# Kernel tuning notes

Measured on AMD Instinct MI355X. Metric: run time of the kernel, lower is better.

The kernel has to match this reference:

```python
import jax, jax.numpy as jnp
import numpy as np

PATCH = 16      # sqrt(n_patches=256)
ALPHA = 10.0
HEADS, DH = 2, 64


def _fourier(coords, Bm):
    # coords: (HW, 2), Bm: (n_features, 2) -> (HW, 2*n_features)
    proj = 2.0 * jnp.pi * coords @ Bm.T
    return jnp.concatenate([jnp.cos(proj), jnp.sin(proj)], axis=-1)


def _forward(coords_decoding, tokens, B_q, B_l0, B_l1,
             qW, qb, toqW, tokvW, tooW, toob,
             bwW0, bwb0, bwW1, bwb1,
             modW0, modb0, modW1, modb1,
             hvW0, hvb0, outW0, outb0, outW1, outb1):
    B = coords_decoding.shape[0]
    Hh, Ww = coords_decoding.shape[1], coords_decoding.shape[2]
    coords = coords_decoding.reshape(B, -1, coords_decoding.shape[-1])
    grid = coords[0]                      # (HW, 2); coords_modulation is None -> same grid
    HW = grid.shape[0]
    m = tokens.shape[1]

    # patch indices and spatial bias
    row = jnp.clip((grid[:, 0] * PATCH).astype(jnp.int32), 0, PATCH - 1)
    col = jnp.clip((grid[:, 1] * PATCH).astype(jnp.int32), 0, PATCH - 1)
    idx = row * PATCH + col               # (HW,)
    t = idx.astype(jnp.float32) / (PATCH * PATCH)
    pos = (jnp.arange(m, dtype=jnp.float32) + 0.5) / m
    rel = -ALPHA * jnp.abs(t[None, :] - pos[:, None]) ** 2   # (m, HW)
    bias = rel.T                          # (HW, m), broadcast over batch & heads

    # query features (shared across batch)
    xq = jax.nn.relu(_fourier(grid, B_q) @ qW + qb)           # (HW, hd)
    xq_b = jnp.broadcast_to(xq[None], (B, HW, xq.shape[-1]))

    # cross attention with spatial bias
    q = (xq_b @ toqW).reshape(B, HW, HEADS, DH).transpose(0, 2, 1, 3)   # (B,h,HW,Dh)
    kv = tokens @ tokvW                                                  # (B,m,2*inner)
    k, v = jnp.split(kv, 2, axis=-1)
    k = k.reshape(B, m, HEADS, DH).transpose(0, 2, 1, 3)                 # (B,h,m,Dh)
    v = v.reshape(B, m, HEADS, DH).transpose(0, 2, 1, 3)
    sim = jnp.einsum('bhqd,bhkd->bhqk', q, k) * (DH ** -0.5) + bias[None, None]
    attn = jax.nn.softmax(sim, axis=-1)
    o = jnp.einsum('bhqk,bhkd->bhqd', attn, v)
    o = o.transpose(0, 2, 1, 3).reshape(B, HW, HEADS * DH)
    mod = o @ tooW + toob                                                # (B,HW,hd)

    # per-band MLP stack (layer_num = 2)
    def band(Bl, bwW, bwb, mW, mb):
        h = jax.nn.relu(_fourier(grid, Bl) @ bwW + bwb)                  # (HW,hd)
        return jax.nn.relu(h[None] + mod @ mW + mb)                      # (B,HW,hd)

    m0 = band(B_l0, bwW0, bwb0, modW0, modb0)
    m1 = band(B_l1, bwW1, bwb1, modW1, modb1)
    hv0 = m0
    hv1 = jax.nn.relu((m1 + hv0) @ hvW0 + hvb0)
    out = (hv0 @ outW0 + outb0) + (hv1 @ outW1 + outb1)                  # (B,HW,3)
    return out.reshape(B, Hh, Ww, -1)


def setup_inputs() -> dict:
    key = jax.random.key(0)
    ks = jax.random.split(key, 32)
    B, H, W, L = 4, 128, 128, 256
    fd, hd, cd, od = 64, 256, 256, 3
    nf = fd // 2
    inner = HEADS * DH

    def lin(k, i, o):
        return jax.random.normal(k, (i, o), dtype=jnp.float32) / np.sqrt(i).astype(np.float32)

    inp = {}
    inp['coords_decoding'] = jax.random.uniform(ks[0], (B, H, W, 2), dtype=jnp.float32)
    inp['tokens'] = jax.random.normal(ks[1], (B, L, cd), dtype=jnp.float32)
    inp['B_q'] = jax.random.normal(ks[2], (nf, 2), dtype=jnp.float32) / 16.0
    inp['B_l0'] = jax.random.normal(ks[3], (nf, 2), dtype=jnp.float32) / 128.0
    inp['B_l1'] = jax.random.normal(ks[4], (nf, 2), dtype=jnp.float32) / 32.0
    inp['qW'] = lin(ks[5], fd, hd); inp['qb'] = jnp.zeros((hd,), jnp.float32)
    inp['toqW'] = lin(ks[6], hd, inner)
    inp['tokvW'] = lin(ks[7], cd, inner * 2)
    inp['tooW'] = lin(ks[8], inner, hd); inp['toob'] = jnp.zeros((hd,), jnp.float32)
    inp['bwW0'] = lin(ks[9], fd, hd); inp['bwb0'] = jnp.zeros((hd,), jnp.float32)
    inp['bwW1'] = lin(ks[10], fd, hd); inp['bwb1'] = jnp.zeros((hd,), jnp.float32)
    inp['modW0'] = lin(ks[11], hd, hd); inp['modb0'] = jnp.zeros((hd,), jnp.float32)
    inp['modW1'] = lin(ks[12], hd, hd); inp['modb1'] = jnp.zeros((hd,), jnp.float32)
    inp['hvW0'] = lin(ks[13], hd, hd); inp['hvb0'] = jnp.zeros((hd,), jnp.float32)
    inp['outW0'] = lin(ks[14], hd, od); inp['outb0'] = jnp.zeros((od,), jnp.float32)
    inp['outW1'] = lin(ks[15], hd, od); inp['outb1'] = jnp.zeros((od,), jnp.float32)
    return inp


def reference(coords_decoding, tokens, B_q, B_l0, B_l1,
              qW, qb, toqW, tokvW, tooW, toob,
              bwW0, bwb0, bwW1, bwb1,
              modW0, modb0, modW1, modb1,
              hvW0, hvb0, outW0, outb0, outW1, outb1):
    return _forward(coords_decoding, tokens, B_q, B_l0, B_l1,
                    qW, qb, toqW, tokvW, tooW, toob,
                    bwW0, bwb0, bwW1, bwb1,
                    modW0, modb0, modW1, modb1,
                    hvW0, hvb0, outW0, outb0, outW1, outb1)
```

## Files before the change

### kernel.cpp

```cpp
#include <hip/hip_runtime.h>
#include <stdint.h>

constexpr int kHW = 16384;
constexpr int kB  = 4;
constexpr int kM  = 256;

typedef _Float16 half8 __attribute__((ext_vector_type(8)));
typedef __attribute__((ext_vector_type(4))) float f32x4;

__device__ __forceinline__ unsigned short f2h(float f) {
  _Float16 h = (_Float16)f;
  return __builtin_bit_cast(unsigned short, h);
}
__device__ __forceinline__ float h2f(unsigned short u) {
  return (float)__builtin_bit_cast(_Float16, u);
}

__global__ __launch_bounds__(256) void prep_kernel(
    const float* __restrict__ tokens, const float* __restrict__ tokvW,
    unsigned short* __restrict__ kn_ws, unsigned short* __restrict__ vt_ws,
    const float* __restrict__ tooW, const float* __restrict__ modW0,
    const float* __restrict__ modW1, const float* __restrict__ hvW0,
    const float* __restrict__ qW, const float* __restrict__ bwW0,
    const float* __restrict__ bwW1, const float* __restrict__ toqW,
    unsigned short* __restrict__ tooWt, unsigned short* __restrict__ modW0t,
    unsigned short* __restrict__ modW1t, unsigned short* __restrict__ hvW0t,
    unsigned short* __restrict__ qWt, unsigned short* __restrict__ bw0t,
    unsigned short* __restrict__ bw1t, unsigned short* __restrict__ toqWt)
{
  __shared__ __align__(16) float tok[256];
  int bx = blockIdx.x, tid = threadIdx.x;

  if (bx < kB * kM) {
    int b = bx >> 8, j = bx & 255, c = tid;
    tok[c] = tokens[(b * kM + j) * 256 + c];
    __syncthreads();
    float acc = 0.f;
    for (int i4 = 0; i4 < 64; i4++) {
      float4 t4 = *(const float4*)&tok[i4 * 4];
      acc += t4.x * tokvW[(i4*4+0)*256 + c] + t4.y * tokvW[(i4*4+1)*256 + c]
           + t4.z * tokvW[(i4*4+2)*256 + c] + t4.w * tokvW[(i4*4+3)*256 + c];
    }
    unsigned short hv = f2h(acc);
    if (c < 128) {
      int h = c >> 6, dd = c & 63;
      kn_ws[((size_t)(b*2+h)*256 + j) * 64 + dd] = hv;
    } else {
      int c2 = c - 128;
      int h = c2 >> 6, dd = c2 & 63;
      vt_ws[((size_t)(b*2+h)*64 + dd) * 256 + j] = hv;
    }
  } else {
    int t = bx - kB * kM;
    int m = t >> 3, ch = t & 7;
    const float* Ws[8] = {tooW, modW0, modW1, hvW0, qW, bwW0, bwW1, toqW};
    unsigned short* Wts[8] = {tooWt, modW0t, modW1t, hvW0t, qWt, bw0t, bw1t, toqWt};
    const int Ks[8] = {128, 256, 256, 256, 64, 64, 64, 256};
    const int Ns[8] = {256, 256, 256, 256, 256, 256, 256, 128};
    const float* W = Ws[m];
    unsigned short* Wt = Wts[m];
    int K = Ks[m], N = Ns[m];
    int nkb = K / 8;
    int per = nkb >> 3;
    int kb0 = ch * per;
    if (tid < N) {
      for (int kb = kb0; kb < kb0 + per; kb++) {
        unsigned short sv[8];
#pragma unroll
        for (int i = 0; i < 8; i++)
          sv[i] = f2h(W[(kb * 8 + i) * N + tid]);
        *(uint4*)&Wt[tid * K + kb * 8] = *(const uint4*)sv;
      }
    }
  }
}

constexpr int kAPitch = 264;
constexpr int kQPitch = 136;

__global__ __launch_bounds__(256, 2) void featattn_kernel(
    const float* __restrict__ coords,
    const float* __restrict__ Bq, const float* __restrict__ Bl0, const float* __restrict__ Bl1,
    const float* __restrict__ qb, const float* __restrict__ bwb0, const float* __restrict__ bwb1,
    const unsigned short* __restrict__ qWt, const unsigned short* __restrict__ bw0t,
    const unsigned short* __restrict__ bw1t, const unsigned short* __restrict__ toqWt,
    const unsigned short* __restrict__ kn_ws, const unsigned short* __restrict__ vt_ws,
    unsigned short* __restrict__ h0_hf, unsigned short* __restrict__ h1_hf,
    unsigned short* __restrict__ o_hf)
{
  __shared__ __align__(16) unsigned short arena[15360];
  __shared__ __align__(16) unsigned short qc_s[32 * kQPitch];
  __shared__ float t_s[32];
  __shared__ float coords_s[64];
  __shared__ float red_max[32][4];
  __shared__ float red_sum[32][4];

  unsigned short* ff  = arena;
  unsigned short* xq  = arena + 6912;
  unsigned short* P_s = arena;

  int tid = threadIdx.x;
  int px0 = blockIdx.x * 32;
  int w = tid >> 6, ln = tid & 63;
  int c = ln & 15, q = ln >> 4;

  const f32x4 zero4 = {0.f, 0.f, 0.f, 0.f};

  if (tid < 64) coords_s[tid] = coords[px0 * 2 + tid];
  __syncthreads();

#pragma unroll
  for (int r = 0; r < 24; r++) {
    int v = r * 256 + tid;
    int mat = v >> 11;
    int p = (v >> 6) & 31;
    int f = v & 63;
    int fr = f & 31;
    const float* Bm = (mat == 0) ? Bq : (mat == 1 ? Bl0 : Bl1);
    float x = coords_s[p * 2 + 0];
    float y = coords_s[p * 2 + 1];
    float proj = 6.283185307179586f * (x * Bm[fr*2+0] + y * Bm[fr*2+1]);
    float s, cc;
    __sincosf(proj, &s, &cc);
    ff[(mat * 32 + p) * 72 + f] = f2h((f < 32) ? cc : s);
  }
  if (tid < 32) {
    float x = coords_s[tid * 2 + 0];
    float y = coords_s[tid * 2 + 1];
    int row = min(max((int)(x * 16.0f), 0), 15);
    int col = min(max((int)(y * 16.0f), 0), 15);
    t_s[tid] = (float)(row * 16 + col) * (1.0f / 256.0f);
  }
  __syncthreads();

  for (int mat = 0; mat < 3; mat++) {
    const unsigned short* Wt = (mat == 0) ? qWt : (mat == 1 ? bw0t : bw1t);
    const float* bias = (mat == 0) ? qb : (mat == 1 ? bwb0 : bwb1);
    f32x4 acc[8];
#pragma unroll
    for (int i = 0; i < 8; i++) acc[i] = zero4;
#pragma unroll
    for (int ks = 0; ks < 2; ks++) {
      int koff = ks * 32 + q * 8;
      half8 bfr[4];
#pragma unroll
      for (int nt = 0; nt < 4; nt++)
        bfr[nt] = *(const half8*)(Wt + (size_t)(w*64 + nt*16 + c) * 64 + koff);
      half8 afr[2];
#pragma unroll
      for (int mt = 0; mt < 2; mt++)
        afr[mt] = *(const half8*)(ff + (mat * 32 + mt*16 + c) * 72 + koff);
#pragma unroll
      for (int mt = 0; mt < 2; mt++)
#pragma unroll
        for (int nt = 0; nt < 4; nt++)
          acc[mt*4+nt] = __builtin_amdgcn_mfma_f32_16x16x32_f16(afr[mt], bfr[nt], acc[mt*4+nt], 0, 0, 0);
    }
    float bv[4];
#pragma unroll
    for (int nt = 0; nt < 4; nt++) bv[nt] = bias[w*64 + nt*16 + c];
#pragma unroll
    for (int mt = 0; mt < 2; mt++)
#pragma unroll
      for (int nt = 0; nt < 4; nt++)
#pragma unroll
        for (int rg = 0; rg < 4; rg++) {
          int row = mt*16 + q*4 + rg, col = w*64 + nt*16 + c;
          unsigned short hv = f2h(fmaxf(acc[mt*4+nt][rg] + bv[nt], 0.f));
          if (mat == 0)      xq[row * kAPitch + col] = hv;
          else if (mat == 1) h0_hf[((size_t)(px0 + row)) * 256 + col] = hv;
          else               h1_hf[((size_t)(px0 + row)) * 256 + col] = hv;
        }
  }
  __syncthreads();

  {
    f32x4 acc2[4];
#pragma unroll
    for (int i = 0; i < 4; i++) acc2[i] = zero4;
#pragma unroll
    for (int kt = 0; kt < 8; kt++) {
      int koff = kt * 32 + q * 8;
      half8 bfr[2];
#pragma unroll
      for (int nt = 0; nt < 2; nt++)
        bfr[nt] = *(const half8*)(toqWt + (size_t)(w*32 + nt*16 + c) * 256 + koff);
      half8 afr[2];
#pragma unroll
      for (int mt = 0; mt < 2; mt++)
        afr[mt] = *(const half8*)(xq + (mt*16 + c) * kAPitch + koff);
#pragma unroll
      for (int mt = 0; mt < 2; mt++)
#pragma unroll
        for (int nt = 0; nt < 2; nt++)
          acc2[mt*2+nt] = __builtin_amdgcn_mfma_f32_16x16x32_f16(afr[mt], bfr[nt], acc2[mt*2+nt], 0, 0, 0);
    }
#pragma unroll
    for (int mt = 0; mt < 2; mt++)
#pragma unroll
      for (int nt = 0; nt < 2; nt++)
#pragma unroll
        for (int rg = 0; rg < 4; rg++) {
          int row = mt*16 + q*4 + rg, col = w*32 + nt*16 + c;
          qc_s[row * kQPitch + col] = f2h(acc2[mt*2+nt][rg]);
        }
  }

  for (int b = 0; b < kB; b++) {
    for (int h = 0; h < 2; h++) {
      __syncthreads();

      f32x4 acc[8];
#pragma unroll
      for (int i = 0; i < 8; i++) acc[i] = zero4;
      const unsigned short* kbase = kn_ws + (size_t)(b*2+h) * 256 * 64;
#pragma unroll
      for (int ks = 0; ks < 2; ks++) {
        int koff = ks * 32 + q * 8;
        half8 a0 = *(const half8*)(qc_s + c * kQPitch + h*64 + koff);
        half8 a1 = *(const half8*)(qc_s + (16 + c) * kQPitch + h*64 + koff);
#pragma unroll
        for (int nt = 0; nt < 4; nt++) {
          half8 bf = *(const half8*)(kbase + (size_t)(w*64 + nt*16 + c) * 64 + koff);
          acc[0*4+nt] = __builtin_amdgcn_mfma_f32_16x16x32_f16(a0, bf, acc[0*4+nt], 0, 0, 0);
          acc[1*4+nt] = __builtin_amdgcn_mfma_f32_16x16x32_f16(a1, bf, acc[1*4+nt], 0, 0, 0);
        }
      }

      float lm[2][4];
#pragma unroll
      for (int mt = 0; mt < 2; mt++)
#pragma unroll
        for (int rg = 0; rg < 4; rg++) {
          int row = mt*16 + q*4 + rg;
          float tv = t_s[row];
          float mx = -1e30f;
#pragma unroll
          for (int nt = 0; nt < 4; nt++) {
            int token = w*64 + nt*16 + c;
            float pos = ((float)token + 0.5f) * (1.0f / 256.0f);
            float db = tv - pos;
            float sb = acc[mt*4+nt][rg] * 0.125f - 10.0f * db * db;
            acc[mt*4+nt][rg] = sb;
            mx = fmaxf(mx, sb);
          }
          lm[mt][rg] = mx;
        }
#pragma unroll
      for (int s = 1; s < 16; s <<= 1)
#pragma unroll
        for (int mt = 0; mt < 2; mt++)
#pragma unroll
          for (int rg = 0; rg < 4; rg++)
            lm[mt][rg] = fmaxf(lm[mt][rg], __shfl_xor(lm[mt][rg], s, 64));
      if (c == 0) {
#pragma unroll
        for (int mt = 0; mt < 2; mt++)
#pragma unroll
          for (int rg = 0; rg < 4; rg++)
            red_max[mt*16 + q*4 + rg][w] = lm[mt][rg];
      }
      __syncthreads();

      float ps[2][4];
#pragma unroll
      for (int mt = 0; mt < 2; mt++)
#pragma unroll
        for (int rg = 0; rg < 4; rg++) {
          int row = mt*16 + q*4 + rg;
          float gm = fmaxf(fmaxf(red_max[row][0], red_max[row][1]),
                           fmaxf(red_max[row][2], red_max[row][3]));
          float sum = 0.f;
#pragma unroll
          for (int nt = 0; nt < 4; nt++) {
            float e = __expf(acc[mt*4+nt][rg] - gm);
            sum += e;
            P_s[row * kAPitch + w*64 + nt*16 + c] = f2h(e);
          }
          ps[mt][rg] = sum;
        }
#pragma unroll
      for (int s = 1; s < 16; s <<= 1)
#pragma unroll
        for (int mt = 0; mt < 2; mt++)
#pragma unroll
          for (int rg = 0; rg < 4; rg++)
            ps[mt][rg] += __shfl_xor(ps[mt][rg], s, 64);
      if (c == 0) {
#pragma unroll
        for (int mt = 0; mt < 2; mt++)
#pragma unroll
          for (int rg = 0; rg < 4; rg++)
            red_sum[mt*16 + q*4 + rg][w] = ps[mt][rg];
      }
      __syncthreads();

      f32x4 oacc[2] = {zero4, zero4};
      const unsigned short* vbase = vt_ws + (size_t)(b*2+h) * 64 * 256;
#pragma unroll
      for (int kt = 0; kt < 8; kt++) {
        int koff = kt * 32 + q * 8;
        half8 bf = *(const half8*)(vbase + (size_t)(w*16 + c) * 256 + koff);
        half8 a0 = *(const half8*)(P_s + (0*16 + c) * kAPitch + koff);
        half8 a1 = *(const half8*)(P_s + (1*16 + c) * kAPitch + koff);
        oacc[0] = __builtin_amdgcn_mfma_f32_16x16x32_f16(a0, bf, oacc[0], 0, 0, 0);
        oacc[1] = __builtin_amdgcn_mfma_f32_16x16x32_f16(a1, bf, oacc[1], 0, 0, 0);
      }
#pragma unroll
      for (int mt = 0; mt < 2; mt++)
#pragma unroll
        for (int rg = 0; rg < 4; rg++) {
          int row = mt*16 + q*4 + rg;
          float rinv = 1.0f / (red_sum[row][0] + red_sum[row][1] +
                               red_sum[row][2] + red_sum[row][3]);
          o_hf[((size_t)(b * kHW + px0 + row)) * 128 + h*64 + w*16 + c] =
              f2h(oacc[mt][rg] * rinv);
        }
    }
  }
}

constexpr int kPitch = 264;

template <int KD>
__device__ __forceinline__ void gemm4(
    const unsigned short* abuf, const unsigned short* wt,
    f32x4* acc , int c, int q)
{
#pragma unroll
  for (int ks = 0; ks < KD / 32; ks++) {
    int koff = ks * 32 + q * 8;
    half8 bfr[4];
#pragma unroll
    for (int nt = 0; nt < 4; nt++)
      bfr[nt] = *(const half8*)(wt + (nt * 16 + c) * KD + koff);
    half8 afr[4];
#pragma unroll
    for (int mt = 0; mt < 4; mt++)
      afr[mt] = *(const half8*)(abuf + (mt * 16 + c) * kPitch + koff);
#pragma unroll
    for (int mt = 0; mt < 4; mt++)
#pragma unroll
      for (int nt = 0; nt < 4; nt++)
        acc[mt * 4 + nt] = __builtin_amdgcn_mfma_f32_16x16x32_f16(afr[mt], bfr[nt], acc[mt * 4 + nt], 0, 0, 0);
  }
}

__global__ __launch_bounds__(256, 2) void mlp_kernel(
    const unsigned short* __restrict__ o_hf,
    const unsigned short* __restrict__ h0_hf, const unsigned short* __restrict__ h1_hf,
    const unsigned short* __restrict__ tooWt, const float* __restrict__ toob,
    const unsigned short* __restrict__ modW0t, const float* __restrict__ modb0,
    const unsigned short* __restrict__ modW1t, const float* __restrict__ modb1,
    const unsigned short* __restrict__ hvW0t, const float* __restrict__ hvb0,
    const float* __restrict__ outW0, const float* __restrict__ outb0,
    const float* __restrict__ outW1, const float* __restrict__ outb1,
    float* __restrict__ dout)
{
  __shared__ __align__(16) unsigned short buf0[64 * kPitch];
  __shared__ __align__(16) unsigned short buf1[64 * kPitch];
  __shared__ __align__(16) float scratch[64 * 12];

  int tid = threadIdx.x;
  int px0 = blockIdx.x * 16;
  int w = tid >> 6, ln = tid & 63;
  int c = ln & 15, q = ln >> 4;

  unsigned short h0r[4][4], h1r[4][4];
#pragma unroll
  for (int nt = 0; nt < 4; nt++) {
    int col = w * 64 + nt * 16 + c;
#pragma unroll
    for (int rg = 0; rg < 4; rg++) {
      int px = q * 4 + rg;
      h0r[nt][rg] = h0_hf[((size_t)(px0 + px)) * 256 + col];
      h1r[nt][rg] = h1_hf[((size_t)(px0 + px)) * 256 + col];
    }
  }

#pragma unroll
  for (int i = 0; i < 4; i++) {
    int idx = i * 256 + tid;
    int r = idx >> 4, c8 = (idx & 15) * 8;
    int b = r >> 4, px = r & 15;
    uint4 v = *(const uint4*)(o_hf + ((size_t)(b * kHW + px0 + px)) * 128 + c8);
    *(uint4*)&buf0[r * kPitch + c8] = v;
  }
  __syncthreads();

  f32x4 acc[16];
  const f32x4 zero4 = {0.f, 0.f, 0.f, 0.f};

#pragma unroll
  for (int i = 0; i < 16; i++) acc[i] = zero4;
  gemm4<128>(buf0, tooWt + (size_t)w * 64 * 128, acc, c, q);
  {
    float bias[4];
#pragma unroll
    for (int nt = 0; nt < 4; nt++) bias[nt] = toob[w * 64 + nt * 16 + c];
#pragma unroll
    for (int mt = 0; mt < 4; mt++)
#pragma unroll
      for (int nt = 0; nt < 4; nt++)
#pragma unroll
        for (int rg = 0; rg < 4; rg++) {
          int row = mt * 16 + q * 4 + rg, col = w * 64 + nt * 16 + c;
          buf1[row * kPitch + col] = f2h(acc[mt * 4 + nt][rg] + bias[nt]);
        }
  }
  __syncthreads();

  _Float16 m0h[4][4][4];
#pragma unroll
  for (int i = 0; i < 16; i++) acc[i] = zero4;
  gemm4<256>(buf1, modW0t + (size_t)w * 64 * 256, acc, c, q);
  {
    float bias[4];
#pragma unroll
    for (int nt = 0; nt < 4; nt++) bias[nt] = modb0[w * 64 + nt * 16 + c];
#pragma unroll
    for (int mt = 0; mt < 4; mt++)
#pragma unroll
      for (int nt = 0; nt < 4; nt++)
#pragma unroll
        for (int rg = 0; rg < 4; rg++)
          m0h[mt][nt][rg] =
              (_Float16)fmaxf(acc[mt * 4 + nt][rg] + bias[nt] + h2f(h0r[nt][rg]), 0.f);
  }

#pragma unroll
  for (int i = 0; i < 16; i++) acc[i] = zero4;
  gemm4<256>(buf1, modW1t + (size_t)w * 64 * 256, acc, c, q);
  {
    float bias[4];
#pragma unroll
    for (int nt = 0; nt < 4; nt++) bias[nt] = modb1[w * 64 + nt * 16 + c];
#pragma unroll
    for (int mt = 0; mt < 4; mt++)
#pragma unroll
      for (int nt = 0; nt < 4; nt++)
#pragma unroll
        for (int rg = 0; rg < 4; rg++) {
          int row = mt * 16 + q * 4 + rg, col = w * 64 + nt * 16 + c;
          float m0v = (float)m0h[mt][nt][rg];
          float v = m0v + fmaxf(acc[mt * 4 + nt][rg] + bias[nt] + h2f(h1r[nt][rg]), 0.f);
          buf0[row * kPitch + col] = f2h(v);
        }
  }
  __syncthreads();

#pragma unroll
  for (int i = 0; i < 16; i++) acc[i] = zero4;
  gemm4<256>(buf0, hvW0t + (size_t)w * 64 * 256, acc, c, q);
  {
    float bias[4], w0v[4][3], w1v[4][3];
#pragma unroll
    for (int nt = 0; nt < 4; nt++) {
      int col = w * 64 + nt * 16 + c;
      bias[nt] = hvb0[col];
#pragma unroll
      for (int k = 0; k < 3; k++) {
        w0v[nt][k] = outW0[col * 3 + k];
        w1v[nt][k] = outW1[col * 3 + k];
      }
    }
#pragma unroll
    for (int mt = 0; mt < 4; mt++) {
      float pk[4][3];
#pragma unroll
      for (int rg = 0; rg < 4; rg++)
#pragma unroll
        for (int k = 0; k < 3; k++) pk[rg][k] = 0.f;
#pragma unroll
      for (int nt = 0; nt < 4; nt++) {
#pragma unroll
        for (int rg = 0; rg < 4; rg++) {
          float hv1 = fmaxf(acc[mt * 4 + nt][rg] + bias[nt], 0.f);
          float m0v = (float)m0h[mt][nt][rg];
#pragma unroll
          for (int k = 0; k < 3; k++)
            pk[rg][k] += m0v * w0v[nt][k] + hv1 * w1v[nt][k];
        }
      }
#pragma unroll
      for (int s = 1; s < 16; s <<= 1)
#pragma unroll
        for (int rg = 0; rg < 4; rg++)
#pragma unroll
          for (int k = 0; k < 3; k++)
            pk[rg][k] += __shfl_xor(pk[rg][k], s, 64);
      if (c == 0) {
#pragma unroll
        for (int rg = 0; rg < 4; rg++) {
          int row = mt * 16 + q * 4 + rg;
#pragma unroll
          for (int k = 0; k < 3; k++)
            scratch[row * 12 + k * 4 + w] = pk[rg][k];
        }
      }
    }
  }
  __syncthreads();

  if (tid < 192) {
    int row = tid / 3, k = tid % 3;
    int b = row >> 4, px = px0 + (row & 15);
    float s = outb0[k] + outb1[k];
#pragma unroll
    for (int ww = 0; ww < 4; ww++) s += scratch[row * 12 + k * 4 + ww];
    dout[((size_t)b * kHW + px) * 3 + k] = s;
  }
}

extern "C" void kernel_launch(void* const* d_in, const int* in_sizes, int n_in,
                              void* d_out, int out_size, void* d_ws, size_t ws_size,
                              hipStream_t stream) {
  const float* coords = (const float*)d_in[0];
  const float* tokens = (const float*)d_in[1];
  const float* Bq     = (const float*)d_in[2];
  const float* Bl0    = (const float*)d_in[3];
  const float* Bl1    = (const float*)d_in[4];
  const float* qW     = (const float*)d_in[5];
  const float* qb     = (const float*)d_in[6];
  const float* toqW   = (const float*)d_in[7];
  const float* tokvW  = (const float*)d_in[8];
  const float* tooW   = (const float*)d_in[9];
  const float* toob   = (const float*)d_in[10];
  const float* bwW0   = (const float*)d_in[11];
  const float* bwb0   = (const float*)d_in[12];
  const float* bwW1   = (const float*)d_in[13];
  const float* bwb1   = (const float*)d_in[14];
  const float* modW0  = (const float*)d_in[15];
  const float* modb0  = (const float*)d_in[16];
  const float* modW1  = (const float*)d_in[17];
  const float* modb1  = (const float*)d_in[18];
  const float* hvW0   = (const float*)d_in[19];
  const float* hvb0   = (const float*)d_in[20];
  const float* outW0  = (const float*)d_in[21];
  const float* outb0  = (const float*)d_in[22];
  const float* outW1  = (const float*)d_in[23];
  const float* outb1  = (const float*)d_in[24];

  char* ws = (char*)d_ws;
  unsigned short* h0_hf  = (unsigned short*)(ws + 0);
  unsigned short* h1_hf  = (unsigned short*)(ws + 8388608);
  unsigned short* o_hf   = (unsigned short*)(ws + 16777216);
  unsigned short* kn_ws  = (unsigned short*)(ws + 33554432);
  unsigned short* vt_ws  = (unsigned short*)(ws + 33816576);
  unsigned short* tooWt  = (unsigned short*)(ws + 34078720);
  unsigned short* modW0t = (unsigned short*)(ws + 34144256);
  unsigned short* modW1t = (unsigned short*)(ws + 34275328);
  unsigned short* hvW0t  = (unsigned short*)(ws + 34406400);
  unsigned short* qWt    = (unsigned short*)(ws + 34537472);
  unsigned short* bw0t   = (unsigned short*)(ws + 34570240);
  unsigned short* bw1t   = (unsigned short*)(ws + 34603008);
  unsigned short* toqWt  = (unsigned short*)(ws + 34635776);

  prep_kernel<<<dim3(kB * kM + 64), 256, 0, stream>>>(
      tokens, tokvW, kn_ws, vt_ws,
      tooW, modW0, modW1, hvW0, qW, bwW0, bwW1, toqW,
      tooWt, modW0t, modW1t, hvW0t, qWt, bw0t, bw1t, toqWt);
  featattn_kernel<<<dim3(kHW / 32), 256, 0, stream>>>(
      coords, Bq, Bl0, Bl1, qb, bwb0, bwb1,
      qWt, bw0t, bw1t, toqWt,
      kn_ws, vt_ws,
      h0_hf, h1_hf, o_hf);
  mlp_kernel<<<dim3(kHW / 16), 256, 0, stream>>>(
      o_hf, h0_hf, h1_hf, tooWt, toob, modW0t, modb0, modW1t, modb1,
      hvW0t, hvb0, outW0, outb0, outW1, outb1, (float*)d_out);
}
```

Measured before the change: 258.8 us.

## Halve MLP kernel row tile and stage residuals in shared memory for occupancy

The MLP kernel now handles 8 pixels (32 rows across the batch) per block instead of 16, so each wave keeps 8 accumulators instead of 16. The h0/h1 residual inputs move from register arrays to a shared buffer, and the m0 intermediate is kept in shared memory instead of registers. Launch bounds rise to 4 blocks per CU and the grid doubles. The goal is to cut register and LDS pressure so more waves run at once. The cost is that each weight tile is read from global/L2 twice as often overall, and the kernel adds extra barriers and more LDS traffic.

Result: slower. 286.9 us (+10.9%).

```diff
diff --git a/kernel.cpp b/kernel.cpp
--- a/kernel.cpp
+++ b/kernel.cpp
@@ -323,7 +323,7 @@
 constexpr int kPitch = 264;
 
 template <int KD>
-__device__ __forceinline__ void gemm4(
+__device__ __forceinline__ void gemm2m(
     const unsigned short* abuf, const unsigned short* wt,
     f32x4* acc , int c, int q)
 {
@@ -334,19 +334,19 @@
 #pragma unroll
     for (int nt = 0; nt < 4; nt++)
       bfr[nt] = *(const half8*)(wt + (nt * 16 + c) * KD + koff);
-    half8 afr[4];
-#pragma unroll
-    for (int mt = 0; mt < 4; mt++)
+    half8 afr[2];
+#pragma unroll
+    for (int mt = 0; mt < 2; mt++)
       afr[mt] = *(const half8*)(abuf + (mt * 16 + c) * kPitch + koff);
 #pragma unroll
-    for (int mt = 0; mt < 4; mt++)
+    for (int mt = 0; mt < 2; mt++)
 #pragma unroll
       for (int nt = 0; nt < 4; nt++)
         acc[mt * 4 + nt] = __builtin_amdgcn_mfma_f32_16x16x32_f16(afr[mt], bfr[nt], acc[mt * 4 + nt], 0, 0, 0);
   }
 }
 
-__global__ __launch_bounds__(256, 2) void mlp_kernel(
+__global__ __launch_bounds__(256, 4) void mlp_kernel(
     const unsigned short* __restrict__ o_hf,
     const unsigned short* __restrict__ h0_hf, const unsigned short* __restrict__ h1_hf,
     const unsigned short* __restrict__ tooWt, const float* __restrict__ toob,
@@ -357,49 +357,43 @@
     const float* __restrict__ outW1, const float* __restrict__ outb1,
     float* __restrict__ dout)
 {
-  __shared__ __align__(16) unsigned short buf0[64 * kPitch];
-  __shared__ __align__(16) unsigned short buf1[64 * kPitch];
-  __shared__ __align__(16) float scratch[64 * 12];
+  __shared__ __align__(16) unsigned short buf0[32 * kPitch];
+  __shared__ __align__(16) unsigned short buf1[32 * kPitch];
+  __shared__ __align__(16) unsigned short hbuf[8 * kPitch];
+  __shared__ __align__(16) float scratch[32 * 12];
 
   int tid = threadIdx.x;
-  int px0 = blockIdx.x * 16;
+  int px0 = blockIdx.x * 8;
   int w = tid >> 6, ln = tid & 63;
   int c = ln & 15, q = ln >> 4;
 
-  unsigned short h0r[4][4], h1r[4][4];
-#pragma unroll
-  for (int nt = 0; nt < 4; nt++) {
-    int col = w * 64 + nt * 16 + c;
-#pragma unroll
-    for (int rg = 0; rg < 4; rg++) {
-      int px = q * 4 + rg;
-      h0r[nt][rg] = h0_hf[((size_t)(px0 + px)) * 256 + col];
-      h1r[nt][rg] = h1_hf[((size_t)(px0 + px)) * 256 + col];
-    }
-  }
-
-#pragma unroll
-  for (int i = 0; i < 4; i++) {
+#pragma unroll
+  for (int i = 0; i < 2; i++) {
     int idx = i * 256 + tid;
     int r = idx >> 4, c8 = (idx & 15) * 8;
-    int b = r >> 4, px = r & 15;
+    int b = r >> 3, px = r & 7;
     uint4 v = *(const uint4*)(o_hf + ((size_t)(b * kHW + px0 + px)) * 128 + c8);
     *(uint4*)&buf0[r * kPitch + c8] = v;
   }
-  __syncthreads();
-
-  f32x4 acc[16];
+  {
+    int p = tid >> 5, c8 = (tid & 31) * 8;
+    uint4 v = *(const uint4*)(h0_hf + ((size_t)(px0 + p)) * 256 + c8);
+    *(uint4*)&hbuf[p * kPitch + c8] = v;
+  }
+  __syncthreads();
+
+  f32x4 acc[8];
   const f32x4 zero4 = {0.f, 0.f, 0.f, 0.f};
 
 #pragma unroll
-  for (int i = 0; i < 16; i++) acc[i] = zero4;
-  gemm4<128>(buf0, tooWt + (size_t)w * 64 * 128, acc, c, q);
+  for (int i = 0; i < 8; i++) acc[i] = zero4;
+  gemm2m<128>(buf0, tooWt + (size_t)w * 64 * 128, acc, c, q);
   {
     float bias[4];
 #pragma unroll
     for (int nt = 0; nt < 4; nt++) bias[nt] = toob[w * 64 + nt * 16 + c];
 #pragma unroll
-    for (int mt = 0; mt < 4; mt++)
+    for (int mt = 0; mt < 2; mt++)
 #pragma unroll
       for (int nt = 0; nt < 4; nt++)
 #pragma unroll
@@ -410,48 +404,68 @@
   }
   __syncthreads();
 
-  _Float16 m0h[4][4][4];
-#pragma unroll
-  for (int i = 0; i < 16; i++) acc[i] = zero4;
-  gemm4<256>(buf1, modW0t + (size_t)w * 64 * 256, acc, c, q);
-  {
-    float bias[4];
-#pragma unroll
-    for (int nt = 0; nt < 4; nt++) bias[nt] = modb0[w * 64 + nt * 16 + c];
-#pragma unroll
-    for (int mt = 0; mt < 4; mt++)
+#pragma unroll
+  for (int i = 0; i < 8; i++) acc[i] = zero4;
+  gemm2m<256>(buf1, modW0t + (size_t)w * 64 * 256, acc, c, q);
+  {
+    float bias[4], hr[4][4];
+#pragma unroll
+    for (int nt = 0; nt < 4; nt++) {
+      int col = w * 64 + nt * 16 + c;
+      bias[nt] = modb0[col];
+#pragma unroll
+      for (int rg = 0; rg < 4; rg++)
+        hr[nt][rg] = h2f(hbuf[((q * 4 + rg) & 7) * kPitch + col]);
+    }
+#pragma unroll
+    for (int mt = 0; mt < 2; mt++)
 #pragma unroll
       for (int nt = 0; nt < 4; nt++)
 #pragma unroll
-        for (int rg = 0; rg < 4; rg++)
-          m0h[mt][nt][rg] =
-              (_Float16)fmaxf(acc[mt * 4 + nt][rg] + bias[nt] + h2f(h0r[nt][rg]), 0.f);
-  }
-
-#pragma unroll
-  for (int i = 0; i < 16; i++) acc[i] = zero4;
-  gemm4<256>(buf1, modW1t + (size_t)w * 64 * 256, acc, c, q);
-  {
-    float bias[4];
-#pragma unroll
-    for (int nt = 0; nt < 4; nt++) bias[nt] = modb1[w * 64 + nt * 16 + c];
-#pragma unroll
-    for (int mt = 0; mt < 4; mt++)
+        for (int rg = 0; rg < 4; rg++) {
+          int row = mt * 16 + q * 4 + rg, col = w * 64 + nt * 16 + c;
+          buf0[row * kPitch + col] =
+              f2h(fmaxf(acc[mt * 4 + nt][rg] + bias[nt] + hr[nt][rg], 0.f));
+        }
+  }
+  __syncthreads();
+
+  {
+    int p = tid >> 5, c8 = (tid & 31) * 8;
+    uint4 v = *(const uint4*)(h1_hf + ((size_t)(px0 + p)) * 256 + c8);
+    *(uint4*)&hbuf[p * kPitch + c8] = v;
+  }
+#pragma unroll
+  for (int i = 0; i < 8; i++) acc[i] = zero4;
+  gemm2m<256>(buf1, modW1t + (size_t)w * 64 * 256, acc, c, q);
+  __syncthreads();
+  {
+    float bias[4], hr[4][4];
+#pragma unroll
+    for (int nt = 0; nt < 4; nt++) {
+      int col = w * 64 + nt * 16 + c;
+      bias[nt] = modb1[col];
+#pragma unroll
+      for (int rg = 0; rg < 4; rg++)
+        hr[nt][rg] = h2f(hbuf[((q * 4 + rg) & 7) * kPitch + col]);
+    }
+#pragma unroll
+    for (int mt = 0; mt < 2; mt++)
 #pragma unroll
       for (int nt = 0; nt < 4; nt++)
 #pragma unroll
         for (int rg = 0; rg < 4; rg++) {
           int row = mt * 16 + q * 4 + rg, col = w * 64 + nt * 16 + c;
-          float m0v = (float)m0h[mt][nt][rg];
-          float v = m0v + fmaxf(acc[mt * 4 + nt][rg] + bias[nt] + h2f(h1r[nt][rg]), 0.f);
-          buf0[row * kPitch + col] = f2h(v);
-        }
-  }
-  __syncthreads();
-
-#pragma unroll
-  for (int i = 0; i < 16; i++) acc[i] = zero4;
-  gemm4<256>(buf0, hvW0t + (size_t)w * 64 * 256, acc, c, q);
+          float m0v = h2f(buf0[row * kPitch + col]);
+          float v = m0v + fmaxf(acc[mt * 4 + nt][rg] + bias[nt] + hr[nt][rg], 0.f);
+          buf1[row * kPitch + col] = f2h(v);
+        }
+  }
+  __syncthreads();
+
+#pragma unroll
+  for (int i = 0; i < 8; i++) acc[i] = zero4;
+  gemm2m<256>(buf1, hvW0t + (size_t)w * 64 * 256, acc, c, q);
   {
     float bias[4], w0v[4][3], w1v[4][3];
 #pragma unroll
@@ -465,7 +479,7 @@
       }
     }
 #pragma unroll
-    for (int mt = 0; mt < 4; mt++) {
+    for (int mt = 0; mt < 2; mt++) {
       float pk[4][3];
 #pragma unroll
       for (int rg = 0; rg < 4; rg++)
@@ -473,10 +487,12 @@
         for (int k = 0; k < 3; k++) pk[rg][k] = 0.f;
 #pragma unroll
       for (int nt = 0; nt < 4; nt++) {
-#pragma unroll
-        for (int rg = 0; rg < 4; rg++) {
+        int col = w * 64 + nt * 16 + c;
+#pragma unroll
+        for (int rg = 0; rg < 4; rg++) {
+          int row = mt * 16 + q * 4 + rg;
           float hv1 = fmaxf(acc[mt * 4 + nt][rg] + bias[nt], 0.f);
-          float m0v = (float)m0h[mt][nt][rg];
+          float m0v = h2f(buf0[row * kPitch + col]);
 #pragma unroll
           for (int k = 0; k < 3; k++)
             pk[rg][k] += m0v * w0v[nt][k] + hv1 * w1v[nt][k];
@@ -502,9 +518,9 @@
   }
   __syncthreads();
 
-  if (tid < 192) {
+  if (tid < 96) {
     int row = tid / 3, k = tid % 3;
-    int b = row >> 4, px = px0 + (row & 15);
+    int b = row >> 3, px = px0 + (row & 7);
     float s = outb0[k] + outb1[k];
 #pragma unroll
     for (int ww = 0; ww < 4; ww++) s += scratch[row * 12 + k * 4 + ww];
@@ -565,7 +581,7 @@
       qWt, bw0t, bw1t, toqWt,
       kn_ws, vt_ws,
       h0_hf, h1_hf, o_hf);
-  mlp_kernel<<<dim3(kHW / 16), 256, 0, stream>>>(
+  mlp_kernel<<<dim3(kHW / 8), 256, 0, stream>>>(
       o_hf, h0_hf, h1_hf, tooWt, toob, modW0t, modb0, modW1t, modb1,
       hvW0t, hvb0, outW0, outb0, outW1, outb1, (float*)d_out);
 }
```
